# Performance work log

Hardware: AMD Instinct MI355X
Metric: run time of the kernel (lower is better)

## Reference

```python
import jax, jax.numpy as jnp
import numpy as np

NUM_ROUTES = 8
TEMPERATURE = 0.1
NEG_INF = -1e9
EPS = 1e-12  # F.normalize eps


def _l2_normalize(t):
    n = jnp.sqrt(jnp.sum(t * t, axis=-1, keepdims=True))
    return t / jnp.maximum(n, EPS)


def setup_inputs() -> dict:
    key = jax.random.key(0)
    ks = jax.random.split(key, 7)
    B, P1, D = 4, 2049, 1024
    s = 1.0 / np.sqrt(D)
    return {
        "x": jax.random.normal(ks[0], (B, P1, D), jnp.float32),
        "Wq": jax.random.normal(ks[1], (D, D), jnp.float32) * s,
        "bq": jax.random.normal(ks[2], (D,), jnp.float32) * 0.01,
        "Wk": jax.random.normal(ks[3], (D, D), jnp.float32) * s,
        "bk": jax.random.normal(ks[4], (D,), jnp.float32) * 0.01,
        "Wv": jax.random.normal(ks[5], (D, D), jnp.float32) * s,
        "bv": jax.random.normal(ks[6], (D,), jnp.float32) * 0.01,
    }


def reference(x, Wq, bq, Wk, bk, Wv, bv):
    x = x[:, 1:, :]  # skip_first=True
    B, P, D = x.shape
    q = _l2_normalize(x @ Wq.T + bq)
    k = _l2_normalize(x @ Wk.T + bk)
    v = x @ Wv.T + bv
    scores = jnp.einsum('bpd,bqd->bpq', q, k)  # [B,P,P]
    diag = jnp.eye(P, dtype=bool)
    scores = jnp.where(diag[None], NEG_INF, scores)
    topk_scores, routes = jax.lax.top_k(scores / TEMPERATURE, NUM_ROUTES)  # [B,P,K]
    weights = jax.nn.softmax(topk_scores, axis=-1)
    b_idx = jnp.arange(B)[:, None, None]
    v_gathered = v[b_idx, routes]  # [B,P,K,D]
    features = jnp.einsum('bpk,bpkd->bpd', weights, v_gathered)
    return routes, weights, features
```

## Files before the change

kernel.cpp:

```cpp
#include <hip/hip_runtime.h>
#include <hip/hip_bf16.h>
#include <math.h>

#define TEMP 0.1
#define NC 10

typedef float f4 __attribute__((ext_vector_type(4)));
typedef short s8v __attribute__((ext_vector_type(8)));
typedef int   i4v __attribute__((ext_vector_type(4)));
typedef _Float16 h8v __attribute__((ext_vector_type(8)));

__device__ inline short f2bf(float f) {
    __hip_bfloat16 h = __float2bfloat16(f);
    return *reinterpret_cast<short*>(&h);
}

__device__ __forceinline__ void g2l16(const void* g, void* l) {
    __builtin_amdgcn_global_load_lds(
        (const __attribute__((address_space(1))) void*)g,
        (__attribute__((address_space(3))) void*)l, 16, 0, 0);
}

__global__ __launch_bounds__(256) void prep_w(
    const float* __restrict__ Wq, const float* __restrict__ Wk,
    const float* __restrict__ Wv,
    signed char* __restrict__ Wql, signed char* __restrict__ Wkl,
    double* __restrict__ wqsc, double* __restrict__ wksc,
    short* __restrict__ Wvh)
{
    const int row = blockIdx.x, tid = threadIdx.x;
    const int which = blockIdx.y;
    if (which == 2) {
        const float4 v = ((const float4*)(Wv + (size_t)row * 1024))[tid];
        __align__(8) short h[4] = {f2bf(v.x), f2bf(v.y), f2bf(v.z), f2bf(v.w)};
        *(short4*)&Wvh[(size_t)row * 1024 + tid * 4] = *(short4*)h;
        return;
    }
    const float* src = which ? Wk : Wq;
    signed char* limbs = which ? Wkl : Wql;
    double* scale = which ? wksc : wqsc;
    const long plane_stride = 1024L * 1024;

    const float4 v = ((const float4*)(src + (size_t)row * 1024))[tid];
    float m = fmaxf(fmaxf(fabsf(v.x), fabsf(v.y)), fmaxf(fabsf(v.z), fabsf(v.w)));
#pragma unroll
    for (int off = 32; off > 0; off >>= 1) m = fmaxf(m, __shfl_down(m, off));
    __shared__ float wmax[4];
    __shared__ int ssig;
    if ((tid & 63) == 0) wmax[tid >> 6] = m;
    __syncthreads();
    if (tid == 0) {
        float rm = fmaxf(fmaxf(wmax[0], wmax[1]), fmaxf(wmax[2], wmax[3]));
        int sig = (rm > 0.f) ? (29 - ilogbf(rm)) : 0;
        ssig = sig;
        scale[row] = ldexp(1.0, -sig);
    }
    __syncthreads();
    const double s2 = ldexp(1.0, ssig);
    float xs[4] = {v.x, v.y, v.z, v.w};
    signed char out[4][4];
#pragma unroll
    for (int e = 0; e < 4; ++e) {
        long X = __double2ll_rn((double)xs[e] * s2);
#pragma unroll
        for (int l = 0; l < 3; ++l) {
            int d = (int)(((X + 128) & 255) - 128);
            out[l][e] = (signed char)d;
            X = (X - d) >> 8;
        }
        out[3][e] = (signed char)X;
    }
#pragma unroll
    for (int l = 0; l < 4; ++l)
        *(char4*)&limbs[(size_t)l * plane_stride + (size_t)row * 1024 + tid * 4] =
            *(char4*)&out[l][0];
}

__global__ __launch_bounds__(256) void prep_x(
    const float* __restrict__ src, signed char* __restrict__ limbs,
    long plane_stride, double* __restrict__ scale,
    short* __restrict__ hi)
{
    const int row = blockIdx.x, tid = threadIdx.x;
    const float4 v = ((const float4*)(src + (size_t)row * 1024))[tid];
    float m = fmaxf(fmaxf(fabsf(v.x), fabsf(v.y)), fmaxf(fabsf(v.z), fabsf(v.w)));
#pragma unroll
    for (int off = 32; off > 0; off >>= 1) m = fmaxf(m, __shfl_down(m, off));
    __shared__ float wmax[4];
    __shared__ int ssig;
    if ((tid & 63) == 0) wmax[tid >> 6] = m;
    __syncthreads();
    if (tid == 0) {
        float rm = fmaxf(fmaxf(wmax[0], wmax[1]), fmaxf(wmax[2], wmax[3]));
        int sig = (rm > 0.f) ? (29 - ilogbf(rm)) : 0;
        ssig = sig;
        scale[row] = ldexp(1.0, -sig);
    }
    __syncthreads();
    const double s2 = ldexp(1.0, ssig);
    float xs[4] = {v.x, v.y, v.z, v.w};
    signed char out[4][4];
    __align__(8) short h[4];
#pragma unroll
    for (int e = 0; e < 4; ++e) {
        long X = __double2ll_rn((double)xs[e] * s2);
#pragma unroll
        for (int lmb = 0; lmb < 3; ++lmb) {
            int d = (int)(((X + 128) & 255) - 128);
            out[lmb][e] = (signed char)d;
            X = (X - d) >> 8;
        }
        out[3][e] = (signed char)X;
        h[e] = f2bf(xs[e]);
    }
#pragma unroll
    for (int lmb = 0; lmb < 4; ++lmb)
        *(char4*)&limbs[(size_t)lmb * plane_stride + (size_t)row * 1024 + tid * 4] =
            *(char4*)&out[lmb][0];
    *(short4*)&hi[(size_t)row * 1024 + tid * 4] = *(short4*)h;
}

__global__ __launch_bounds__(256, 4) void gemm_i8qk(
    const signed char* __restrict__ Xl,
    const signed char* __restrict__ Wql,
    const signed char* __restrict__ Wkl,
    const double* __restrict__ xsc,
    const double* __restrict__ wqsc, const double* __restrict__ wksc,
    const float* __restrict__ bq, const float* __restrict__ bk,
    float* __restrict__ Qf, float* __restrict__ Kf)
{
    const int K = 1024, N = 1024;
    const long MK = 2048L * 1024, NK = 1024L * 1024;
    const signed char* Wl = blockIdx.z ? Wkl : Wql;
    const double* wsc = blockIdx.z ? wksc : wqsc;
    const float* bias = blockIdx.z ? bk : bq;
    float* C = blockIdx.z ? Kf : Qf;

    __shared__ __align__(16) signed char Asm[4][64][64];
    __shared__ __align__(16) signed char Bsm[4][64][64];

    const int tid  = threadIdx.x;
    const int lane = tid & 63, wave = tid >> 6;
    const int wm = wave >> 1, wn = wave & 1;
    const int quad = lane >> 4, l16 = lane & 15;
    const int m0 = blockIdx.y * 64, n0 = blockIdx.x * 64;

    const int srow = tid >> 2;
    const int cswz = ((tid & 3) ^ ((srow >> 1) & 3));
    const signed char* ap = Xl + (size_t)(m0 + srow) * K + cswz * 16;
    const signed char* bp = Wl + (size_t)(n0 + srow) * K + cswz * 16;

    signed char* aw = (signed char*)Asm + (wave << 10);
    signed char* bw = (signed char*)Bsm + (wave << 10);

    i4v acc[4][2][2] = {};

    for (int k0 = 0; k0 < K; k0 += 64) {
        __syncthreads();
#pragma unroll
        for (int l = 0; l < 4; ++l) {
            g2l16(ap + l * MK + k0, aw + l * 4096);
            g2l16(bp + l * NK + k0, bw + l * 4096);
        }
        __syncthreads();

        i4v bF[4][2];
#pragma unroll
        for (int j = 0; j < 4; ++j)
#pragma unroll
            for (int nt = 0; nt < 2; ++nt) {
                const int R = wn * 32 + nt * 16 + l16;
                bF[j][nt] = *(const i4v*)&Bsm[j][R][(quad ^ ((R >> 1) & 3)) * 16];
            }

#pragma unroll
        for (int i = 0; i < 4; ++i) {
            const int R0 = wm * 32 + l16;
            const int R1 = wm * 32 + 16 + l16;
            i4v a0 = *(const i4v*)&Asm[i][R0][(quad ^ ((R0 >> 1) & 3)) * 16];
            i4v a1 = *(const i4v*)&Asm[i][R1][(quad ^ ((R1 >> 1) & 3)) * 16];
#pragma unroll
            for (int j = 0; j < 4; ++j) {
                if (i + j < 3) continue;
                const int s = i + j - 3;
                acc[s][0][0] = __builtin_amdgcn_mfma_i32_16x16x64_i8(a0, bF[j][0], acc[s][0][0], 0, 0, 0);
                acc[s][0][1] = __builtin_amdgcn_mfma_i32_16x16x64_i8(a0, bF[j][1], acc[s][0][1], 0, 0, 0);
                acc[s][1][0] = __builtin_amdgcn_mfma_i32_16x16x64_i8(a1, bF[j][0], acc[s][1][0], 0, 0, 0);
                acc[s][1][1] = __builtin_amdgcn_mfma_i32_16x16x64_i8(a1, bF[j][1], acc[s][1][1], 0, 0, 0);
            }
        }
    }

    const double wt0 = ldexp(1.0, 24), wt1 = ldexp(1.0, 32);
    const double wt2 = ldexp(1.0, 40), wt3 = ldexp(1.0, 48);
#pragma unroll
    for (int mt = 0; mt < 2; ++mt)
#pragma unroll
        for (int nt = 0; nt < 2; ++nt)
#pragma unroll
            for (int r = 0; r < 4; ++r) {
                int row = m0 + wm * 32 + mt * 16 + quad * 4 + r;
                int col = n0 + wn * 32 + nt * 16 + l16;
                double dsum = wt0 * (double)acc[0][mt][nt][r]
                            + wt1 * (double)acc[1][mt][nt][r]
                            + wt2 * (double)acc[2][mt][nt][r]
                            + wt3 * (double)acc[3][mt][nt][r];
                C[(size_t)row * N + col] =
                    (float)(dsum * xsc[row] * wsc[col] + (double)bias[col]);
            }
}

__global__ __launch_bounds__(256, 4) void gemm_v64(
    const short* __restrict__ Ahp, const short* __restrict__ Bhp,
    const float* __restrict__ bias, float* __restrict__ C)
{
    const int K = 1024, N = 1024;
    __shared__ __align__(16) short Ah[64][32];
    __shared__ __align__(16) short Bh[64][32];

    const int tid = threadIdx.x, lane = tid & 63, wave = tid >> 6;
    const int wm = wave >> 1, wn = wave & 1;
    const int quad = lane >> 4, l16 = lane & 15;
    const int m0 = blockIdx.y * 64, n0 = blockIdx.x * 64;
    const int srow = tid >> 2;
    const int cswz = ((tid & 3) ^ ((srow >> 1) & 3));
    const char* ap = (const char*)(Ahp + (size_t)(m0 + srow) * K) + cswz * 16;
    const char* bp = (const char*)(Bhp + (size_t)(n0 + srow) * K) + cswz * 16;
    char* aw = (char*)Ah + (wave << 10);
    char* bw = (char*)Bh + (wave << 10);

    f4 acc[2][2] = {};
    for (int k0 = 0; k0 < K; k0 += 32) {
        __syncthreads();
        g2l16(ap + 2 * k0, aw);
        g2l16(bp + 2 * k0, bw);
        __syncthreads();

        s8v af[2], bf[2];
#pragma unroll
        for (int t = 0; t < 2; ++t) {
            const int Ra = wm * 32 + t * 16 + l16;
            const int Rb = wn * 32 + t * 16 + l16;
            af[t] = *(const s8v*)((const char*)Ah + Ra * 64 + ((quad ^ ((Ra >> 1) & 3)) << 4));
            bf[t] = *(const s8v*)((const char*)Bh + Rb * 64 + ((quad ^ ((Rb >> 1) & 3)) << 4));
        }
#pragma unroll
        for (int mt = 0; mt < 2; ++mt)
#pragma unroll
            for (int nt = 0; nt < 2; ++nt)
                acc[mt][nt] = __builtin_amdgcn_mfma_f32_16x16x32_bf16(
                    af[mt], bf[nt], acc[mt][nt], 0, 0, 0);
    }
#pragma unroll
    for (int mt = 0; mt < 2; ++mt)
#pragma unroll
        for (int nt = 0; nt < 2; ++nt)
#pragma unroll
            for (int r = 0; r < 4; ++r) {
                int row = m0 + wm * 32 + mt * 16 + quad * 4 + r;
                int col = n0 + wn * 32 + nt * 16 + l16;
                C[(size_t)row * N + col] = acc[mt][nt][r] + bias[col];
            }
}

__global__ __launch_bounds__(256, 4) void gemm_score(
    const short* __restrict__ Qh, const short* __restrict__ Kh,
    float* __restrict__ C)
{
    const int K = 1024, N = 2048;
    __shared__ __align__(16) short As[64][32];
    __shared__ __align__(16) short Bs[64][32];
    const int tid = threadIdx.x, lane = tid & 63, wave = tid >> 6;
    const int wm = wave >> 1, wn = wave & 1;
    const int quad = lane >> 4, l16 = lane & 15;
    const int m0 = blockIdx.y * 64, n0 = blockIdx.x * 64;
    const int srow = tid >> 2;
    const int cswz = ((tid & 3) ^ ((srow >> 1) & 3));
    const char* ap = (const char*)(Qh + (size_t)(m0 + srow) * K) + cswz * 16;
    const char* bp = (const char*)(Kh + (size_t)(n0 + srow) * K) + cswz * 16;
    char* aw = (char*)As + (wave << 10);
    char* bw = (char*)Bs + (wave << 10);

    f4 acc[2][2] = {};
    for (int k0 = 0; k0 < K; k0 += 32) {
        __syncthreads();
        g2l16(ap + 2 * k0, aw);
        g2l16(bp + 2 * k0, bw);
        __syncthreads();

        h8v af[2], bf[2];
#pragma unroll
        for (int t = 0; t < 2; ++t) {
            const int Ra = wm * 32 + t * 16 + l16;
            const int Rb = wn * 32 + t * 16 + l16;
            af[t] = *(const h8v*)((const char*)As + Ra * 64 + ((quad ^ ((Ra >> 1) & 3)) << 4));
            bf[t] = *(const h8v*)((const char*)Bs + Rb * 64 + ((quad ^ ((Rb >> 1) & 3)) << 4));
        }
#pragma unroll
        for (int mt = 0; mt < 2; ++mt)
#pragma unroll
            for (int nt = 0; nt < 2; ++nt)
                acc[mt][nt] = __builtin_amdgcn_mfma_f32_16x16x32_f16(
                    af[mt], bf[nt], acc[mt][nt], 0, 0, 0);
    }
#pragma unroll
    for (int mt = 0; mt < 2; ++mt)
#pragma unroll
        for (int nt = 0; nt < 2; ++nt)
#pragma unroll
            for (int r = 0; r < 4; ++r) {
                int row = m0 + wm * 32 + mt * 16 + quad * 4 + r;
                int col = n0 + wn * 32 + nt * 16 + l16;
                C[(size_t)row * N + col] = acc[mt][nt][r];
            }
}

__global__ __launch_bounds__(256) void l2norm_f32h16(
    float* __restrict__ fq, float* __restrict__ fk,
    short* __restrict__ hq, short* __restrict__ hk)
{
    float* f = blockIdx.y ? fk : fq;
    short* h = blockIdx.y ? hk : hq;
    const int row = blockIdx.x;
    const int tid = threadIdx.x;
    float4* p4 = (float4*)(f + (size_t)row * 1024);
    float4 v = p4[tid];
    double s = (double)v.x * v.x + (double)v.y * v.y
             + (double)v.z * v.z + (double)v.w * v.w;
#pragma unroll
    for (int off = 32; off > 0; off >>= 1) s += __shfl_down(s, off);
    __shared__ double ws[5];
    if ((tid & 63) == 0) ws[tid >> 6] = s;
    __syncthreads();
    if (tid == 0) ws[4] = fmax(sqrt(ws[0] + ws[1] + ws[2] + ws[3]), 1e-12);
    __syncthreads();
    const double inv = 1.0 / ws[4];
    float o0 = (float)(v.x * inv), o1 = (float)(v.y * inv);
    float o2 = (float)(v.z * inv), o3 = (float)(v.w * inv);
    float4 o = make_float4(o0, o1, o2, o3);
    p4[tid] = o;
    __align__(8) _Float16 hv[4] = {(_Float16)o0, (_Float16)o1,
                                   (_Float16)o2, (_Float16)o3};
    *(short4*)&h[(size_t)row * 1024 + tid * 4] = *(short4*)hv;
}

__global__ __launch_bounds__(256) void topk_route(
    const float*  __restrict__ S,
    const float*  __restrict__ Qf,
    const float*  __restrict__ Kf,
    const float*  __restrict__ Vf,
    float* __restrict__ routes_out,
    float* __restrict__ weights_out,
    float* __restrict__ feat_out,
    int batch)
{
    const int P = 2048, D = 1024;
    __shared__ float  qrow[1024];
    __shared__ float  cval[4 * NC];
    __shared__ int    cidx[4 * NC];
    __shared__ int    sel[NC];
    __shared__ double cscore[NC];
    __shared__ int    topi_s[8];
    __shared__ float  wts[8];

    const int p = blockIdx.x;
    const int tid = threadIdx.x;
    const int lane = tid & 63, wave = tid >> 6;

    const float4* sr4 = (const float4*)(S + (size_t)p * P);
    const float4 s0 = sr4[tid];
    const float4 s1 = sr4[tid + 256];
    ((float4*)qrow)[tid] = ((const float4*)(Qf + (size_t)p * D))[tid];

    float v[8] = {s0.x, s0.y, s0.z, s0.w, s1.x, s1.y, s1.z, s1.w};
    int   ji[8];
#pragma unroll
    for (int e = 0; e < 8; ++e) {
        ji[e] = (e < 4) ? (4 * tid + e) : (1024 + 4 * tid + (e - 4));
        if (ji[e] == p) v[e] = -1e30f;
    }

    float lv = v[0]; int li = ji[0];
#pragma unroll
    for (int e = 1; e < 8; ++e)
        if (v[e] > lv) { lv = v[e]; li = ji[e]; }

    float cv_ = -INFINITY; int ci_ = 0x7fffffff;
#pragma unroll 1
    for (int it = 0; it < NC; ++it) {
        float bv = lv; int bi = li;
#pragma unroll
        for (int off = 32; off > 0; off >>= 1) {
            float ov = __shfl_xor(bv, off);
            int   oi = __shfl_xor(bi, off);
            if (ov > bv || (ov == bv && oi < bi)) { bv = ov; bi = oi; }
        }
        if (lane == it) { cv_ = bv; ci_ = bi; }
#pragma unroll
        for (int e = 0; e < 8; ++e)
            if (ji[e] == bi) v[e] = -INFINITY;
        lv = v[0]; li = ji[0];
#pragma unroll
        for (int e = 1; e < 8; ++e)
            if (v[e] > lv) { lv = v[e]; li = ji[e]; }
    }
    if (lane < NC) { cval[wave * NC + lane] = cv_; cidx[wave * NC + lane] = ci_; }
    __syncthreads();

    if (wave == 0) {
        float mv = (lane < 4 * NC) ? cval[lane] : -INFINITY;
        int   mi = (lane < 4 * NC) ? cidx[lane] : 0x7fffffff;
        int rank = 0;
#pragma unroll 1
        for (int j = 0; j < 4 * NC; ++j) {
            float vj = __shfl(mv, j);
            int   ij = __shfl(mi, j);
            rank += (vj > mv || (vj == mv && ij < mi)) ? 1 : 0;
        }
        if (lane < 4 * NC && rank < NC) sel[rank] = mi;
    }
    __syncthreads();

    float pfv[8];
#pragma unroll
    for (int c = 0; c < 8; ++c)
        pfv[c] = Vf[(size_t)sel[c] * D + tid * 4];

    {
        const float* k0r = Kf + (size_t)sel[wave] * D;
        const float* k1r = Kf + (size_t)sel[wave + 4] * D;
        const float* k2r = Kf + (size_t)sel[8 + (wave & 1)] * D;
        double a0 = 0.0, a1 = 0.0, a2 = 0.0;
#pragma unroll 4
        for (int j = 0; j < 8; ++j) {
            const int e = lane * 2 + j * 128;
            const float2 q2 = *(const float2*)&qrow[e];
            const float2 kA = *(const float2*)&k0r[e];
            const float2 kB = *(const float2*)&k1r[e];
            const float2 kC = *(const float2*)&k2r[e];
            a0 = fma((double)q2.x, (double)kA.x, fma((double)q2.y, (double)kA.y, a0));
            a1 = fma((double)q2.x, (double)kB.x, fma((double)q2.y, (double)kB.y, a1));
            a2 = fma((double)q2.x, (double)kC.x, fma((double)q2.y, (double)kC.y, a2));
        }
#pragma unroll
        for (int off = 32; off > 0; off >>= 1) {
            a0 += __shfl_xor(a0, off);
            a1 += __shfl_xor(a1, off);
            a2 += __shfl_xor(a2, off);
        }
        if (lane == 0) {
            cscore[wave]     = a0;
            cscore[wave + 4] = a1;
            if (wave < 2) cscore[8 + wave] = a2;
        }
    }

    {
        float pf = 0.f;
#pragma unroll
        for (int c = 0; c < 8; ++c) pf += pfv[c];
        asm volatile("" :: "v"(pf));
    }
    __syncthreads();

    if (wave == 0) {
        double sc_ = (lane < NC) ? cscore[lane] : -1.0e308;
        int    id_ = (lane < NC) ? sel[lane]    : 0x7fffffff;
        int rank = 0;
#pragma unroll
        for (int j = 0; j < NC; ++j) {
            double vj = __shfl(sc_, j);
            int    ij = __shfl(id_, j);
            rank += (vj > sc_ || (vj == sc_ && ij < id_)) ? 1 : 0;
        }
        double mm = sc_;
#pragma unroll
        for (int off = 32; off > 0; off >>= 1) mm = fmax(mm, __shfl_xor(mm, off));
        double e = (rank < 8 && lane < NC) ? exp((sc_ - mm) / TEMP) : 0.0;
        double sum = e;
#pragma unroll
        for (int off = 32; off > 0; off >>= 1) sum += __shfl_xor(sum, off);
        if (rank < 8 && lane < NC) {
            float wk = (float)(e / sum);
            wts[rank] = wk; topi_s[rank] = id_;
            const size_t row = (size_t)batch * P + p;
            routes_out[row * 8 + rank]  = (float)id_;
            weights_out[row * 8 + rank] = wk;
        }
    }
    __syncthreads();

    float4 a = {0.f, 0.f, 0.f, 0.f};
#pragma unroll
    for (int k = 0; k < 8; ++k) {
        const float4 v4 = ((const float4*)(Vf + (size_t)topi_s[k] * D))[tid];
        float wk = wts[k];
        a.x = fmaf(wk, v4.x, a.x);
        a.y = fmaf(wk, v4.y, a.y);
        a.z = fmaf(wk, v4.z, a.z);
        a.w = fmaf(wk, v4.w, a.w);
    }
    ((float4*)(feat_out + ((size_t)batch * P + p) * D))[tid] = a;
}

extern "C" void kernel_launch(void* const* d_in, const int* in_sizes, int n_in,
                              void* d_out, int out_size, void* d_ws, size_t ws_size,
                              hipStream_t stream)
{
    const float* x  = (const float*)d_in[0];
    const float* Wq = (const float*)d_in[1];
    const float* bq = (const float*)d_in[2];
    const float* Wk = (const float*)d_in[3];
    const float* bk = (const float*)d_in[4];
    const float* Wv = (const float*)d_in[5];
    const float* bv = (const float*)d_in[6];

    const int B = 4, P = 2048, D = 1024;
    const size_t PD = (size_t)P * D;
    const size_t DD = (size_t)D * D;

    float*  Qf   = (float*)d_ws;
    float*  Kf   = Qf + PD;
    double* xsc  = (double*)(Kf + PD);
    double* wqsc = xsc + 2048;
    double* wksc = wqsc + 1024;
    short*  Qh   = (short*)(wksc + 1024);
    short*  Kh   = Qh + PD;
    short*  xh   = Kh + PD;
    short*  Wvh  = xh + PD;
    float*  Vf   = (float*)(Wvh + DD);
    float*  Sf   = Vf + PD;
    signed char* Xl  = (signed char*)(Sf + (size_t)P * P);
    signed char* Wql = Xl + 4 * PD;
    signed char* Wkl = Wql + 4 * DD;

    float* out     = (float*)d_out;
    float* routes  = out;
    float* weights = out + (size_t)B * P * 8;
    float* feat    = out + (size_t)B * P * 16;

    dim3 blk(256);
    prep_w<<<dim3(1024, 3), blk, 0, stream>>>(Wq, Wk, Wv, Wql, Wkl, wqsc, wksc, Wvh);

    for (int b = 0; b < B; ++b) {
        const float* xb = x + ((size_t)b * 2049 + 1) * D;
        prep_x<<<dim3(P), blk, 0, stream>>>(xb, Xl, (long)PD, xsc, xh);
        gemm_i8qk<<<dim3(16, 32, 2), blk, 0, stream>>>(Xl, Wql, Wkl, xsc, wqsc, wksc,
                                                       bq, bk, Qf, Kf);
        gemm_v64<<<dim3(16, 32), blk, 0, stream>>>(xh, Wvh, bv, Vf);
        l2norm_f32h16<<<dim3(P, 2), blk, 0, stream>>>(Qf, Kf, Qh, Kh);
        gemm_score<<<dim3(32, 32), blk, 0, stream>>>(Qh, Kh, Sf);
        topk_route<<<dim3(P), blk, 0, stream>>>(Sf, Qf, Kf, Vf, routes, weights, feat, b);
    }
}
```

Baseline: 629.4 us.

## Fuse Q and K int8 limb GEMMs into one block sharing the X tile

Each block now computes both the Q and K projection tiles, loading the X limb tile into LDS once and reusing its fragments for both weight matrices. The grid drops its z dimension, halving the number of blocks. Accumulator registers double, so launch bounds are relaxed from 4 to 2 blocks per SM. This trades lower occupancy and a smaller grid for less global/LDS traffic on the shared A operand.

After: 599.7 us, median of 2. 4.7% less time.

```diff
diff --git a/kernel.cpp b/kernel.cpp
--- a/kernel.cpp
+++ b/kernel.cpp
@@ -120,7 +120,7 @@
     *(short4*)&hi[(size_t)row * 1024 + tid * 4] = *(short4*)h;
 }
 
-__global__ __launch_bounds__(256, 4) void gemm_i8qk(
+__global__ __launch_bounds__(256, 2) void gemm_i8qk(
     const signed char* __restrict__ Xl,
     const signed char* __restrict__ Wql,
     const signed char* __restrict__ Wkl,
@@ -131,13 +131,10 @@
 {
     const int K = 1024, N = 1024;
     const long MK = 2048L * 1024, NK = 1024L * 1024;
-    const signed char* Wl = blockIdx.z ? Wkl : Wql;
-    const double* wsc = blockIdx.z ? wksc : wqsc;
-    const float* bias = blockIdx.z ? bk : bq;
-    float* C = blockIdx.z ? Kf : Qf;
 
     __shared__ __align__(16) signed char Asm[4][64][64];
-    __shared__ __align__(16) signed char Bsm[4][64][64];
+    __shared__ __align__(16) signed char Bqm[4][64][64];
+    __shared__ __align__(16) signed char Bkm[4][64][64];
 
     const int tid  = threadIdx.x;
     const int lane = tid & 63, wave = tid >> 6;
@@ -147,46 +144,61 @@
 
     const int srow = tid >> 2;
     const int cswz = ((tid & 3) ^ ((srow >> 1) & 3));
-    const signed char* ap = Xl + (size_t)(m0 + srow) * K + cswz * 16;
-    const signed char* bp = Wl + (size_t)(n0 + srow) * K + cswz * 16;
-
-    signed char* aw = (signed char*)Asm + (wave << 10);
-    signed char* bw = (signed char*)Bsm + (wave << 10);
-
-    i4v acc[4][2][2] = {};
+    const signed char* ap  = Xl  + (size_t)(m0 + srow) * K + cswz * 16;
+    const signed char* bqp = Wql + (size_t)(n0 + srow) * K + cswz * 16;
+    const signed char* bkp = Wkl + (size_t)(n0 + srow) * K + cswz * 16;
+
+    signed char* aw  = (signed char*)Asm + (wave << 10);
+    signed char* bqw = (signed char*)Bqm + (wave << 10);
+    signed char* bkw = (signed char*)Bkm + (wave << 10);
+
+    i4v accq[4][2][2] = {};
+    i4v acck[4][2][2] = {};
+
+    const int R0  = wm * 32 + l16;
+    const int R1  = wm * 32 + 16 + l16;
+    const int c0  = (quad ^ ((R0 >> 1) & 3)) * 16;
+    const int c1  = (quad ^ ((R1 >> 1) & 3)) * 16;
+    const int Rn0 = wn * 32 + l16;
+    const int Rn1 = wn * 32 + 16 + l16;
+    const int cn0 = (quad ^ ((Rn0 >> 1) & 3)) * 16;
+    const int cn1 = (quad ^ ((Rn1 >> 1) & 3)) * 16;
 
     for (int k0 = 0; k0 < K; k0 += 64) {
         __syncthreads();
 #pragma unroll
         for (int l = 0; l < 4; ++l) {
-            g2l16(ap + l * MK + k0, aw + l * 4096);
-            g2l16(bp + l * NK + k0, bw + l * 4096);
+            g2l16(ap  + l * MK + k0, aw  + l * 4096);
+            g2l16(bqp + l * NK + k0, bqw + l * 4096);
+            g2l16(bkp + l * NK + k0, bkw + l * 4096);
         }
         __syncthreads();
 
-        i4v bF[4][2];
-#pragma unroll
-        for (int j = 0; j < 4; ++j)
-#pragma unroll
-            for (int nt = 0; nt < 2; ++nt) {
-                const int R = wn * 32 + nt * 16 + l16;
-                bF[j][nt] = *(const i4v*)&Bsm[j][R][(quad ^ ((R >> 1) & 3)) * 16];
-            }
-
+        i4v aF0[4], aF1[4];
 #pragma unroll
         for (int i = 0; i < 4; ++i) {
-            const int R0 = wm * 32 + l16;
-            const int R1 = wm * 32 + 16 + l16;
-            i4v a0 = *(const i4v*)&Asm[i][R0][(quad ^ ((R0 >> 1) & 3)) * 16];
-            i4v a1 = *(const i4v*)&Asm[i][R1][(quad ^ ((R1 >> 1) & 3)) * 16];
-#pragma unroll
-            for (int j = 0; j < 4; ++j) {
+            aF0[i] = *(const i4v*)&Asm[i][R0][c0];
+            aF1[i] = *(const i4v*)&Asm[i][R1][c1];
+        }
+
+#pragma unroll
+        for (int j = 0; j < 4; ++j) {
+            i4v bq0 = *(const i4v*)&Bqm[j][Rn0][cn0];
+            i4v bq1 = *(const i4v*)&Bqm[j][Rn1][cn1];
+            i4v bk0 = *(const i4v*)&Bkm[j][Rn0][cn0];
+            i4v bk1 = *(const i4v*)&Bkm[j][Rn1][cn1];
+#pragma unroll
+            for (int i = 0; i < 4; ++i) {
                 if (i + j < 3) continue;
                 const int s = i + j - 3;
-                acc[s][0][0] = __builtin_amdgcn_mfma_i32_16x16x64_i8(a0, bF[j][0], acc[s][0][0], 0, 0, 0);
-                acc[s][0][1] = __builtin_amdgcn_mfma_i32_16x16x64_i8(a0, bF[j][1], acc[s][0][1], 0, 0, 0);
-                acc[s][1][0] = __builtin_amdgcn_mfma_i32_16x16x64_i8(a1, bF[j][0], acc[s][1][0], 0, 0, 0);
-                acc[s][1][1] = __builtin_amdgcn_mfma_i32_16x16x64_i8(a1, bF[j][1], acc[s][1][1], 0, 0, 0);
+                accq[s][0][0] = __builtin_amdgcn_mfma_i32_16x16x64_i8(aF0[i], bq0, accq[s][0][0], 0, 0, 0);
+                accq[s][0][1] = __builtin_amdgcn_mfma_i32_16x16x64_i8(aF0[i], bq1, accq[s][0][1], 0, 0, 0);
+                accq[s][1][0] = __builtin_amdgcn_mfma_i32_16x16x64_i8(aF1[i], bq0, accq[s][1][0], 0, 0, 0);
+                accq[s][1][1] = __builtin_amdgcn_mfma_i32_16x16x64_i8(aF1[i], bq1, accq[s][1][1], 0, 0, 0);
+                acck[s][0][0] = __builtin_amdgcn_mfma_i32_16x16x64_i8(aF0[i], bk0, acck[s][0][0], 0, 0, 0);
+                acck[s][0][1] = __builtin_amdgcn_mfma_i32_16x16x64_i8(aF0[i], bk1, acck[s][0][1], 0, 0, 0);
+                acck[s][1][0] = __builtin_amdgcn_mfma_i32_16x16x64_i8(aF1[i], bk0, acck[s][1][0], 0, 0, 0);
+                acck[s][1][1] = __builtin_amdgcn_mfma_i32_16x16x64_i8(aF1[i], bk1, acck[s][1][1], 0, 0, 0);
             }
         }
     }
@@ -201,12 +213,19 @@
             for (int r = 0; r < 4; ++r) {
                 int row = m0 + wm * 32 + mt * 16 + quad * 4 + r;
                 int col = n0 + wn * 32 + nt * 16 + l16;
-                double dsum = wt0 * (double)acc[0][mt][nt][r]
-                            + wt1 * (double)acc[1][mt][nt][r]
-                            + wt2 * (double)acc[2][mt][nt][r]
-                            + wt3 * (double)acc[3][mt][nt][r];
-                C[(size_t)row * N + col] =
-                    (float)(dsum * xsc[row] * wsc[col] + (double)bias[col]);
+                const double xr = xsc[row];
+                double dq = wt0 * (double)accq[0][mt][nt][r]
+                          + wt1 * (double)accq[1][mt][nt][r]
+                          + wt2 * (double)accq[2][mt][nt][r]
+                          + wt3 * (double)accq[3][mt][nt][r];
+                Qf[(size_t)row * N + col] =
+                    (float)(dq * xr * wqsc[col] + (double)bq[col]);
+                double dk = wt0 * (double)acck[0][mt][nt][r]
+                          + wt1 * (double)acck[1][mt][nt][r]
+                          + wt2 * (double)acck[2][mt][nt][r]
+                          + wt3 * (double)acck[3][mt][nt][r];
+                Kf[(size_t)row * N + col] =
+                    (float)(dk * xr * wksc[col] + (double)bk[col]);
             }
 }
 
@@ -545,8 +564,8 @@
     for (int b = 0; b < B; ++b) {
         const float* xb = x + ((size_t)b * 2049 + 1) * D;
         prep_x<<<dim3(P), blk, 0, stream>>>(xb, Xl, (long)PD, xsc, xh);
-        gemm_i8qk<<<dim3(16, 32, 2), blk, 0, stream>>>(Xl, Wql, Wkl, xsc, wqsc, wksc,
-                                                       bq, bk, Qf, Kf);
+        gemm_i8qk<<<dim3(16, 32), blk, 0, stream>>>(Xl, Wql, Wkl, xsc, wqsc, wksc,
+                                                    bq, bk, Qf, Kf);
         gemm_v64<<<dim3(16, 32), blk, 0, stream>>>(xh, Wvh, bv, Vf);
         l2norm_f32h16<<<dim3(P, 2), blk, 0, stream>>>(Qf, Kf, Qh, Kh);
         gemm_score<<<dim3(32, 32), blk, 0, stream>>>(Qh, Kh, Sf);
```
